# Performance work log

Measured on AMD Instinct MI355X. Metric: run time of the kernel, lower is better.

Reference implementation:

```python
import jax, jax.numpy as jnp
import numpy as np


def setup_inputs() -> dict:
    key = jax.random.key(0)
    k1, k2, k3, k4 = jax.random.split(key, 4)
    b_, c_in, T, n, ks, c_out = 32, 32, 12, 1024, 3, 64
    x = jax.random.normal(k1, (b_, c_in, T, n), dtype=jnp.float32)
    Lk = jax.random.normal(k2, (ks, n, n), dtype=jnp.float32) / np.sqrt(n)
    theta = jax.random.normal(k3, (c_in, c_out, ks), dtype=jnp.float32) * 0.05
    b = jax.random.normal(k4, (1, c_out, 1, 1), dtype=jnp.float32) * 0.05
    return {"x": x, "Lk": Lk, "theta": theta, "b": b}


def reference(x, Lk, theta, b):
    # x: (B, c_in, T, N); Lk: (ks, N, N); theta: (c_in, c_out, ks); b: (1, c_out, 1, 1)
    c_in = x.shape[1]
    c_out = theta.shape[1]
    # Chebyshev graph convolution
    x_c = jnp.einsum('knm,bitm->bitkn', Lk, x)          # (B, c_in, T, ks, N)
    x_gc = jnp.einsum('iok,bitkn->botn', theta, x_c) + b  # (B, c_out, T, N)
    # Align: c_in (32) < c_out (64) -> zero-pad channel dim
    x_in = jnp.pad(x, ((0, 0), (0, c_out - c_in), (0, 0), (0, 0)))
    return jax.nn.relu(x_gc + x_in)
```

## Files before the change

kernel.cpp:

```cpp
#include <hip/hip_runtime.h>
#include <hip/hip_bf16.h>


typedef __attribute__((ext_vector_type(8))) short s16x8;
typedef __attribute__((ext_vector_type(4))) float f32x4;
typedef __attribute__((ext_vector_type(4))) float fvec4;

__device__ __forceinline__ short f2bf(float f) {
    union { float f; unsigned u; } v; v.f = f;
    unsigned r = v.u + 0x7fffu + ((v.u >> 16) & 1u);
    return (short)(r >> 16);
}

#define U1 1572864
#define U2 393216
#define U3 6144
__global__ __launch_bounds__(256) void prep_k(const float* __restrict__ x,
                                              const float* __restrict__ Lk,
                                              const float* __restrict__ th,
                                              short* __restrict__ xb,
                                              short* __restrict__ lbT,
                                              short* __restrict__ thb) {
    int gid = blockIdx.x * 256 + threadIdx.x;
    if (gid < U1) {
        const fvec4* s4 = (const fvec4*)x;
        fvec4 a = s4[2 * gid], b = s4[2 * gid + 1];
        s16x8 o;
        o[0]=f2bf(a[0]); o[1]=f2bf(a[1]); o[2]=f2bf(a[2]); o[3]=f2bf(a[3]);
        o[4]=f2bf(b[0]); o[5]=f2bf(b[1]); o[6]=f2bf(b[2]); o[7]=f2bf(b[3]);
        ((s16x8*)xb)[gid] = o;
    } else if (gid < U1 + U2) {
        int u = gid - U1;
        int row = u >> 7, m8 = u & 127;
        int n = row / 3, k = row - n * 3;
        const fvec4* s4 = (const fvec4*)(Lk + (k << 20) + n * 1024 + m8 * 8);
        fvec4 a = s4[0], b = s4[1];
        s16x8 o;
        o[0]=f2bf(a[0]); o[1]=f2bf(a[1]); o[2]=f2bf(a[2]); o[3]=f2bf(a[3]);
        o[4]=f2bf(b[0]); o[5]=f2bf(b[1]); o[6]=f2bf(b[2]); o[7]=f2bf(b[3]);
        ((s16x8*)lbT)[row * 128 + m8] = o;
    } else if (gid < U1 + U2 + U3) {
        int e = gid - U1 - U2;
        int i = e / 192, rem = e - i * 192;
        int o = rem / 3, k = rem - o * 3;
        thb[o * 96 + i * 3 + k] = f2bf(th[e]);
    }
}

#define STAGE_A(kstep, j, bufb)                                                 \
    __builtin_amdgcn_global_load_lds(                                           \
        (const __attribute__((address_space(1))) void*)                         \
            (A + a_srcoff[j] + (kstep) * 64),                                   \
        (__attribute__((address_space(3))) void*)                               \
            (&smem[(bufb) * 16384 + (j) * 4096 + w * 512]), 16, 0, 0);

#define STAGE_B(kstep, j, bufb)                                                 \
    __builtin_amdgcn_global_load_lds(                                           \
        (const __attribute__((address_space(1))) void*)                         \
            (Bm + b_srcoff[j] + (kstep) * 64),                                  \
        (__attribute__((address_space(3))) void*)                               \
            (&smem[32768 + (bufb) * 12288 + (j) * 4096 + w * 512]), 16, 0, 0);

#define MFMA12(M0)                                                              \
    __builtin_amdgcn_s_setprio(1);                                              \
    _Pragma("unroll")                                                           \
    for (int mi = 0; mi < 2; ++mi) {                                            \
        _Pragma("unroll")                                                       \
        for (int ni = 0; ni < 3; ++ni) {                                        \
            acc[(M0) + mi][ni] = __builtin_amdgcn_mfma_f32_16x16x32_bf16(       \
                af[mi][0], bfm[ni][0], acc[(M0) + mi][ni], 0, 0, 0);            \
            acc[(M0) + mi][ni] = __builtin_amdgcn_mfma_f32_16x16x32_bf16(       \
                af[mi][1], bfm[ni][1], acc[(M0) + mi][ni], 0, 0, 0);            \
        }                                                                       \
    }                                                                           \
    __builtin_amdgcn_s_setprio(0);

#define WAIT_LGKM()                                                             \
    asm volatile("s_waitcnt lgkmcnt(0)" ::: "memory");                          \
    __builtin_amdgcn_sched_barrier(0);

__global__ __launch_bounds__(512, 2) void fused_k(const short* __restrict__ A,
                                                  const short* __restrict__ Bm,
                                                  const short* __restrict__ thb,
                                                  const float* __restrict__ bias,
                                                  const float* __restrict__ xres,
                                                  float* __restrict__ out) {
    __shared__ short smem[57344];
    const int tid  = threadIdx.x;
    const int lane = tid & 63;
    const int w    = tid >> 6;
    const int wm   = w >> 2, wn = w & 3;

    int bid = blockIdx.x;
    bid = (bid & 7) * 96 + (bid >> 3);
    const int bm = bid >> 4, bn = bid & 15;
    const int g0 = bm * 8;

    const int srow8 = w * 8 + (lane >> 3);
    const int sj_c  = ((lane & 7) ^ (lane >> 3)) * 8;

    int a_srcoff[4];
    #pragma unroll
    for (int j = 0; j < 4; ++j) {
        const int q = j * 64 + srow8;
        const int G = q >> 5, i = q & 31;
        const int g = g0 + G;
        const int b = g / 12, t_ = g - b * 12;
        a_srcoff[j] = (b * 384 + i * 12 + t_) * 1024 + sj_c;
    }
    int b_srcoff[3];
    #pragma unroll
    for (int j = 0; j < 3; ++j)
        b_srcoff[j] = (bn * 192 + j * 64 + srow8) * 1024 + sj_c;

    const int swzc0 = ((((lane >> 4) * 16)) ^ ((lane & 7) << 4)) >> 1;
    const int swzc1 = ((64 + (lane >> 4) * 16) ^ ((lane & 7) << 4)) >> 1;
    const int fr = lane & 15;

    f32x4 acc[8][3] = {};
    s16x8 bfm[3][2];

    STAGE_A(0, 0, 0) STAGE_A(0, 1, 0) STAGE_A(0, 2, 0) STAGE_A(0, 3, 0)
    STAGE_B(0, 0, 0) STAGE_B(0, 1, 0) STAGE_B(0, 2, 0)
    STAGE_B(1, 0, 1) STAGE_B(1, 1, 1) STAGE_B(1, 2, 1)
    asm volatile("s_waitcnt vmcnt(3)" ::: "memory");
    __builtin_amdgcn_s_barrier();

    for (int t = 0; t < 16; ++t) {
        const int buf = t & 1;
        const int abase = buf * 16384;
        const int bbase = 32768 + buf * 12288;
        s16x8 af[2][2];

        #pragma unroll
        for (int ni = 0; ni < 3; ++ni) {
            const int r = wn * 48 + ni * 16 + fr;
            bfm[ni][0] = *(const s16x8*)&smem[bbase + r * 64 + swzc0];
            bfm[ni][1] = *(const s16x8*)&smem[bbase + r * 64 + swzc1];
        }
        #pragma unroll
        for (int mi = 0; mi < 2; ++mi) {
            const int r = wm * 128 + mi * 16 + fr;
            af[mi][0] = *(const s16x8*)&smem[abase + r * 64 + swzc0];
            af[mi][1] = *(const s16x8*)&smem[abase + r * 64 + swzc1];
        }
        if (t + 1 < 16) { STAGE_A(t + 1, 0, buf ^ 1) STAGE_A(t + 1, 1, buf ^ 1) }
        __builtin_amdgcn_s_barrier();
        WAIT_LGKM();
        MFMA12(0);
        __builtin_amdgcn_s_barrier();

        #pragma unroll
        for (int mi = 0; mi < 2; ++mi) {
            const int r = wm * 128 + (mi + 2) * 16 + fr;
            af[mi][0] = *(const s16x8*)&smem[abase + r * 64 + swzc0];
            af[mi][1] = *(const s16x8*)&smem[abase + r * 64 + swzc1];
        }
        if (t + 1 < 16) { STAGE_A(t + 1, 2, buf ^ 1) STAGE_A(t + 1, 3, buf ^ 1) }
        __builtin_amdgcn_s_barrier();
        WAIT_LGKM();
        MFMA12(2);
        __builtin_amdgcn_s_barrier();

        #pragma unroll
        for (int mi = 0; mi < 2; ++mi) {
            const int r = wm * 128 + (mi + 4) * 16 + fr;
            af[mi][0] = *(const s16x8*)&smem[abase + r * 64 + swzc0];
            af[mi][1] = *(const s16x8*)&smem[abase + r * 64 + swzc1];
        }
        if (t + 2 < 16) { STAGE_B(t + 2, 0, buf) STAGE_B(t + 2, 1, buf) }
        __builtin_amdgcn_s_barrier();
        WAIT_LGKM();
        MFMA12(4);
        __builtin_amdgcn_s_barrier();

        #pragma unroll
        for (int mi = 0; mi < 2; ++mi) {
            const int r = wm * 128 + (mi + 6) * 16 + fr;
            af[mi][0] = *(const s16x8*)&smem[abase + r * 64 + swzc0];
            af[mi][1] = *(const s16x8*)&smem[abase + r * 64 + swzc1];
        }
        if (t + 2 < 16) { STAGE_B(t + 2, 2, buf) }
        __builtin_amdgcn_s_barrier();
        WAIT_LGKM();
        MFMA12(6);
        if (t < 14) { asm volatile("s_waitcnt vmcnt(3)" ::: "memory"); }
        else        { asm volatile("s_waitcnt vmcnt(0)" ::: "memory"); }
        __builtin_amdgcn_s_barrier();
    }

    const int rq = (lane >> 4) * 4;
    #pragma unroll
    for (int mi = 0; mi < 8; ++mi) {
        const int G = wm * 4 + (mi >> 1);
        const int ib = (mi & 1) * 16 + rq;
        #pragma unroll
        for (int ni = 0; ni < 3; ++ni) {
            const int c  = wn * 48 + ni * 16 + fr;
            const int nl = c / 3, kk = c - nl * 3;
            const int base = G * 6656 + nl * 104 + kk;
            #pragma unroll
            for (int r = 0; r < 4; ++r)
                smem[base + (ib + r) * 3] = f2bf(acc[mi][ni][r]);
        }
    }
    __syncthreads();

    const int g  = g0 + w;
    const int b  = g / 12, t_ = g - b * 12;
    const int rq8 = (lane >> 4) * 8;
    s16x8 ta[4][3];
    #pragma unroll
    for (int oi = 0; oi < 4; ++oi)
        #pragma unroll
        for (int ks = 0; ks < 3; ++ks)
            ta[oi][ks] = *(const s16x8*)&thb[(oi * 16 + fr) * 96 + ks * 32 + rq8];

    f32x4 a2[4][4] = {};
    #pragma unroll
    for (int nj = 0; nj < 4; ++nj) {
        s16x8 pb[3];
        #pragma unroll
        for (int ks = 0; ks < 3; ++ks)
            pb[ks] = *(const s16x8*)&smem[w * 6656 + (nj * 16 + fr) * 104 + ks * 32 + rq8];
        #pragma unroll
        for (int oi = 0; oi < 4; ++oi)
            #pragma unroll
            for (int ks = 0; ks < 3; ++ks)
                a2[oi][nj] = __builtin_amdgcn_mfma_f32_16x16x32_bf16(
                    ta[oi][ks], pb[ks], a2[oi][nj], 0, 0, 0);
    }

    const int n0 = bn * 64;
    #pragma unroll
    for (int oi = 0; oi < 4; ++oi) {
        #pragma unroll
        for (int nj = 0; nj < 4; ++nj) {
            const int nl = n0 + nj * 16 + fr;
            #pragma unroll
            for (int r = 0; r < 4; ++r) {
                const int o = oi * 16 + rq + r;
                float v = a2[oi][nj][r] + bias[o];
                if (o < 32) v += xres[(b * 384 + o * 12 + t_) * 1024 + nl];
                out[((b * 64 + o) * 12 + t_) * 1024 + nl] = fmaxf(v, 0.f);
            }
        }
    }
}

extern "C" void kernel_launch(void* const* d_in, const int* in_sizes, int n_in,
                              void* d_out, int out_size, void* d_ws, size_t ws_size,
                              hipStream_t stream) {
    const float* x     = (const float*)d_in[0];
    const float* Lk    = (const float*)d_in[1];
    const float* theta = (const float*)d_in[2];
    const float* bias  = (const float*)d_in[3];
    float* out = (float*)d_out;

    char* ws = (char*)d_ws;
    short* xb  = (short*)(ws);
    short* lbT = (short*)(ws + 25165824);
    short* thb = (short*)(ws + 31457280);

    hipLaunchKernelGGL(prep_k,  dim3(7704), dim3(256), 0, stream,
                       x, Lk, theta, xb, lbT, thb);
    hipLaunchKernelGGL(fused_k, dim3(768),  dim3(512), 0, stream,
                       xb, lbT, thb, bias, x, out);
}
```

Measured before the change: 234.5 us.

## Triple-buffer A tiles in LDS and read residual from bf16 copy

The A-operand staging moves from double to triple buffering in LDS, so tiles are prefetched two k-steps ahead. B stays double-buffered, and the vmcnt wait is relaxed to allow more loads in flight. The residual add in the epilogue now reads the bf16 copy of x instead of the fp32 original, which halves those bytes but lowers the residual's precision. The larger LDS footprint (144KB per block) may reduce occupancy, because launch_bounds asks for 2 blocks per CU.

```diff
diff --git a/kernel.cpp b/kernel.cpp
--- a/kernel.cpp
+++ b/kernel.cpp
@@ -10,6 +10,10 @@
     union { float f; unsigned u; } v; v.f = f;
     unsigned r = v.u + 0x7fffu + ((v.u >> 16) & 1u);
     return (short)(r >> 16);
+}
+__device__ __forceinline__ float bf2f(short h) {
+    union { unsigned u; float f; } v; v.u = ((unsigned)(unsigned short)h) << 16;
+    return v.f;
 }
 
 #define U1 1572864
@@ -47,19 +51,19 @@
     }
 }
 
-#define STAGE_A(kstep, j, bufb)                                                 \
+#define STAGE_A(kstep, j, ldsb)                                                 \
     __builtin_amdgcn_global_load_lds(                                           \
         (const __attribute__((address_space(1))) void*)                         \
             (A + a_srcoff[j] + (kstep) * 64),                                   \
         (__attribute__((address_space(3))) void*)                               \
-            (&smem[(bufb) * 16384 + (j) * 4096 + w * 512]), 16, 0, 0);
-
-#define STAGE_B(kstep, j, bufb)                                                 \
+            (&smem[(ldsb) + (j) * 4096 + w * 512]), 16, 0, 0);
+
+#define STAGE_B(kstep, j, ldsb)                                                 \
     __builtin_amdgcn_global_load_lds(                                           \
         (const __attribute__((address_space(1))) void*)                         \
             (Bm + b_srcoff[j] + (kstep) * 64),                                  \
         (__attribute__((address_space(3))) void*)                               \
-            (&smem[32768 + (bufb) * 12288 + (j) * 4096 + w * 512]), 16, 0, 0);
+            (&smem[(ldsb) + (j) * 4096 + w * 512]), 16, 0, 0);
 
 #define MFMA12(M0)                                                              \
     __builtin_amdgcn_s_setprio(1);                                              \
@@ -83,9 +87,8 @@
                                                   const short* __restrict__ Bm,
                                                   const short* __restrict__ thb,
                                                   const float* __restrict__ bias,
-                                                  const float* __restrict__ xres,
                                                   float* __restrict__ out) {
-    __shared__ short smem[57344];
+    __shared__ short smem[73728];
     const int tid  = threadIdx.x;
     const int lane = tid & 63;
     const int w    = tid >> 6;
@@ -120,16 +123,18 @@
     f32x4 acc[8][3] = {};
     s16x8 bfm[3][2];
 
-    STAGE_A(0, 0, 0) STAGE_A(0, 1, 0) STAGE_A(0, 2, 0) STAGE_A(0, 3, 0)
-    STAGE_B(0, 0, 0) STAGE_B(0, 1, 0) STAGE_B(0, 2, 0)
-    STAGE_B(1, 0, 1) STAGE_B(1, 1, 1) STAGE_B(1, 2, 1)
-    asm volatile("s_waitcnt vmcnt(3)" ::: "memory");
+    STAGE_A(0, 0, 0)     STAGE_A(0, 1, 0)     STAGE_A(0, 2, 0)     STAGE_A(0, 3, 0)
+    STAGE_B(0, 0, 49152) STAGE_B(0, 1, 49152) STAGE_B(0, 2, 49152)
+    STAGE_A(1, 0, 16384) STAGE_A(1, 1, 16384) STAGE_A(1, 2, 16384) STAGE_A(1, 3, 16384)
+    STAGE_B(1, 0, 61440) STAGE_B(1, 1, 61440) STAGE_B(1, 2, 61440)
+    asm volatile("s_waitcnt vmcnt(7)" ::: "memory");
     __builtin_amdgcn_s_barrier();
 
+    int rs = 0, ss = 2;
     for (int t = 0; t < 16; ++t) {
-        const int buf = t & 1;
-        const int abase = buf * 16384;
-        const int bbase = 32768 + buf * 12288;
+        const int abase = rs * 16384;
+        const int astg  = ss * 16384;
+        const int bbase = 49152 + (t & 1) * 12288;
         s16x8 af[2][2];
 
         #pragma unroll
@@ -144,7 +149,7 @@
             af[mi][0] = *(const s16x8*)&smem[abase + r * 64 + swzc0];
             af[mi][1] = *(const s16x8*)&smem[abase + r * 64 + swzc1];
         }
-        if (t + 1 < 16) { STAGE_A(t + 1, 0, buf ^ 1) STAGE_A(t + 1, 1, buf ^ 1) }
+        if (t < 14) { STAGE_A(t + 2, 0, astg) STAGE_A(t + 2, 1, astg) }
         __builtin_amdgcn_s_barrier();
         WAIT_LGKM();
         MFMA12(0);
@@ -156,7 +161,7 @@
             af[mi][0] = *(const s16x8*)&smem[abase + r * 64 + swzc0];
             af[mi][1] = *(const s16x8*)&smem[abase + r * 64 + swzc1];
         }
-        if (t + 1 < 16) { STAGE_A(t + 1, 2, buf ^ 1) STAGE_A(t + 1, 3, buf ^ 1) }
+        if (t < 14) { STAGE_A(t + 2, 2, astg) STAGE_A(t + 2, 3, astg) }
         __builtin_amdgcn_s_barrier();
         WAIT_LGKM();
         MFMA12(2);
@@ -168,7 +173,7 @@
             af[mi][0] = *(const s16x8*)&smem[abase + r * 64 + swzc0];
             af[mi][1] = *(const s16x8*)&smem[abase + r * 64 + swzc1];
         }
-        if (t + 2 < 16) { STAGE_B(t + 2, 0, buf) STAGE_B(t + 2, 1, buf) }
+        if (t < 14) { STAGE_B(t + 2, 0, bbase) STAGE_B(t + 2, 1, bbase) }
         __builtin_amdgcn_s_barrier();
         WAIT_LGKM();
         MFMA12(4);
@@ -180,13 +185,15 @@
             af[mi][0] = *(const s16x8*)&smem[abase + r * 64 + swzc0];
             af[mi][1] = *(const s16x8*)&smem[abase + r * 64 + swzc1];
         }
-        if (t + 2 < 16) { STAGE_B(t + 2, 2, buf) }
+        if (t < 14) { STAGE_B(t + 2, 2, bbase) }
         __builtin_amdgcn_s_barrier();
         WAIT_LGKM();
         MFMA12(6);
-        if (t < 14) { asm volatile("s_waitcnt vmcnt(3)" ::: "memory"); }
+        if (t < 14) { asm volatile("s_waitcnt vmcnt(7)" ::: "memory"); }
         else        { asm volatile("s_waitcnt vmcnt(0)" ::: "memory"); }
         __builtin_amdgcn_s_barrier();
+        rs = (rs == 2) ? 0 : rs + 1;
+        ss = (ss == 2) ? 0 : ss + 1;
     }
 
     const int rq = (lane >> 4) * 4;
@@ -241,7 +248,7 @@
             for (int r = 0; r < 4; ++r) {
                 const int o = oi * 16 + rq + r;
                 float v = a2[oi][nj][r] + bias[o];
-                if (o < 32) v += xres[(b * 384 + o * 12 + t_) * 1024 + nl];
+                if (o < 32) v += bf2f(A[(b * 384 + o * 12 + t_) * 1024 + nl]);
                 out[((b * 64 + o) * 12 + t_) * 1024 + nl] = fmaxf(v, 0.f);
             }
         }
@@ -265,5 +272,5 @@
     hipLaunchKernelGGL(prep_k,  dim3(7704), dim3(256), 0, stream,
                        x, Lk, theta, xb, lbT, thb);
     hipLaunchKernelGGL(fused_k, dim3(768),  dim3(512), 0, stream,
-                       xb, lbT, thb, bias, x, out);
-}
+                       xb, lbT, thb, bias, out);
+}
```

After: 228.4 us. 2.6% less time.
